# Kernel optimization log

Measured on AMD Instinct MI355X. Metric: run time of the kernel, lower is better.

The kernel has to match this reference:

```python
import jax, jax.numpy as jnp
import numpy as np

BEV_H = 200
BEV_W = 200
H_METERS = 100.0
W_METERS = 100.0
THRESHOLD = 0.05
LOW_PASS = 0.3  # 3DGS screen-space low-pass filter added to cov2D diagonal
ALPHA_MIN = 1.0 / 255.0
ALPHA_MAX = 0.99


def setup_inputs() -> dict:
    key = jax.random.key(0)
    k1, k2, k3, k4 = jax.random.split(key, 4)
    B, G, D = 2, 2000, 32
    features = jax.random.normal(k1, (B, G, D), dtype=jnp.float32)
    # means uniformly covering the [-50, 50] x [-50, 50] BEV extent (z unused)
    means3D = (jax.random.uniform(k2, (B, G, 3), dtype=jnp.float32) - 0.5) * 100.0
    # PSD 3x3 covariances, ~1-2 m std -> a few pixels at 2 px/m
    A = jax.random.normal(k3, (B, G, 3, 3), dtype=jnp.float32)
    Sigma = jnp.einsum('bgij,bgkj->bgik', A, A) + 0.1 * jnp.eye(3, dtype=jnp.float32)
    iu = jnp.triu_indices(3)
    cov3D = Sigma[:, :, iu[0], iu[1]]  # b g 6 : (xx, xy, xz, yy, yz, zz)
    opacities = jax.random.uniform(k4, (B, G, 1), dtype=jnp.float32)
    return {'features': features, 'means3D': means3D, 'cov3D': cov3D,
            'opacities': opacities}


def _render(features, means3D, cov3D, opacities):
    B, G, D = features.shape
    sh = BEV_H / H_METERS  # 2 px / m
    sw = BEV_W / W_METERS
    op = opacities[..., 0]                      # b g
    mask = op > THRESHOLD                       # opacity gating (torch masks rows;
                                                # zero-alpha is mathematically identical)
    # orthographic BEV projection (full_proj_transform rows 0 and 1)
    x, y = means3D[..., 0], means3D[..., 1]
    u = -sh * y + BEV_H / 2.0                   # row coordinate, b g
    v = -sw * x + BEV_W / 2.0                   # col coordinate, b g
    # cov2D = M Sigma M^T with M = [[0, sh, 0], [sw, 0, 0]], plus low-pass
    sxx, sxy, syy = cov3D[..., 0], cov3D[..., 1], cov3D[..., 3]
    c00 = sh * sh * syy + LOW_PASS
    c01 = sh * sw * sxy
    c11 = sw * sw * sxx + LOW_PASS
    det = c00 * c11 - c01 * c01
    valid = mask & (det > 0.0)
    inv_det = jnp.where(det > 0.0, 1.0 / jnp.where(det > 0.0, det, 1.0), 0.0)
    cA = c11 * inv_det                          # conic (A, B, C)
    cB = -c01 * inv_det
    cC = c00 * inv_det
    # per-pixel Gaussian power, separably broadcast: [b g H 1] + [b g 1 W]
    gi = jnp.arange(BEV_H, dtype=jnp.float32)
    gj = jnp.arange(BEV_W, dtype=jnp.float32)
    du = u[..., None] - gi                      # b g H
    dv = v[..., None] - gj                      # b g W
    power = (-0.5 * cA)[..., None, None] * (du * du)[..., :, None] \
          + (-0.5 * cC)[..., None, None] * (dv * dv)[..., None, :] \
          + (-cB)[..., None, None] * du[..., :, None] * dv[..., None, :]  # b g H W
    alpha = jnp.minimum(ALPHA_MAX, op[..., None, None] * jnp.exp(power))
    keep = valid[..., None, None] & (power <= 0.0) & (alpha >= ALPHA_MIN)
    alpha = jnp.where(keep, alpha, 0.0)
    alpha = alpha.reshape(B, G, BEV_H * BEV_W)  # b g p
    # front-to-back alpha compositing: exclusive cumprod of transmittance
    T_excl = jnp.concatenate(
        [jnp.ones((B, 1, BEV_H * BEV_W), dtype=alpha.dtype),
         jnp.cumprod(1.0 - alpha, axis=1)[:, :-1]], axis=1)
    weight = alpha * T_excl                     # b g p
    out = jnp.einsum('bgp,bgd->bdp', weight, features)  # bg_color is zeros
    out = out.reshape(B, D, BEV_H, BEV_W)
    num_gaussians = jnp.mean(jnp.sum(mask.astype(jnp.float32), axis=1))
    return out, num_gaussians


def reference(features, means3D, cov3D, opacities):
    return _render(features, means3D, cov3D, opacities)
```

## Files before the change

### kernel.cpp

```cpp
#include <hip/hip_runtime.h>
#include <math.h>

#define BEV_H 200
#define BEV_W 200
#define NPIX (BEV_H * BEV_W)
#define TILE 8
#define NT 25
#define NB 2
#define T_DEAD 1e-10f
#define SEGCAP 512
#define PCAP 128
#define KC 32
#define NLOG255 (-5.5412635f)

__device__ __forceinline__ unsigned pk2bf(float x, float y)
{
    unsigned ux = __float_as_uint(x), uy = __float_as_uint(y);
    ux = ux + 0x7fffu + ((ux >> 16) & 1u);
    uy = uy + 0x7fffu + ((uy >> 16) & 1u);
    return (ux >> 16) | (uy & 0xffff0000u);
}

__global__ __launch_bounds__(256, 5) void render_fused_kernel(
    const float* __restrict__ features, const float* __restrict__ means3D,
    const float* __restrict__ cov3D, const float* __restrict__ opac,
    float* __restrict__ out, int G)
{
    __shared__ __align__(16) unsigned char smem[24576];
    unsigned short* glist = (unsigned short*)smem;
    float4* plA = (float4*)(smem + 4096);
    float2* plB = (float2*)(smem + 12288);
    uint4*  flq = (uint4*)(smem + 16384);
    float*  xch = (float*)smem;

    const int tid  = threadIdx.x;
    const int lane = tid & 63;
    const int w    = tid >> 6;
    const int b  = blockIdx.z;
    const int tj = blockIdx.x;
    const int ti = blockIdx.y;
    const int j = tj * TILE + (lane & 7);
    const int i = ti * TILE + (lane >> 3);
    const float fi = (float)i, fj = (float)j;
    const float ti_lo = (float)(ti * TILE), ti_hi = ti_lo + (TILE - 1);
    const float tj_lo = (float)(tj * TILE), tj_hi = tj_lo + (TILE - 1);
    const int gbase = b * G;
    const int g_lo = (w * G) >> 2;
    const int g_hi = ((w + 1) * G) >> 2;
    const int rounds = (g_hi - g_lo + 63) >> 6;

    int tot = 0;
    {
        int gg = min(g_lo + lane, g_hi - 1);
        size_t gi = (size_t)(gbase + gg);
        float x0 = means3D[gi * 3 + 0], y0 = means3D[gi * 3 + 1];
        float s0 = cov3D[gi * 6 + 0], s1 = cov3D[gi * 6 + 1], s3 = cov3D[gi * 6 + 3];
        float o0 = opac[gi];
        for (int r = 0; r < rounds; ++r) {
            float x1 = 0.f, y1 = 0.f, t0 = 0.f, t1 = 0.f, t3 = 0.f, o1 = 0.f;
            if (r + 1 < rounds) {
                const int gn = min(g_lo + (r + 1) * 64 + lane, g_hi - 1);
                const size_t gni = (size_t)(gbase + gn);
                x1 = means3D[gni * 3 + 0]; y1 = means3D[gni * 3 + 1];
                t0 = cov3D[gni * 6 + 0];   t1 = cov3D[gni * 6 + 1];
                t3 = cov3D[gni * 6 + 3];   o1 = opac[gni];
            }
            const int g = g_lo + r * 64 + lane;
            const float u = -2.0f * y0 + 100.0f;
            const float v = -2.0f * x0 + 100.0f;
            const float c00 = 4.0f * s3 + 0.3f;
            const float c01 = 4.0f * s1;
            const float c11 = 4.0f * s0 + 0.3f;
            const float det = c00 * c11 - c01 * c01;
            bool keep = false;
            float L = 0.0f;
            if (o0 > 0.05f && det > 0.0f && g < g_hi) {
                L = __logf(255.0f * o0);
                const float ru = sqrtf(2.0f * L * c00) + 0.01f;
                const float rv = sqrtf(2.0f * L * c11) + 0.01f;
                keep = (u + ru >= ti_lo) && (u - ru <= ti_hi) &&
                       (v + rv >= tj_lo) && (v - rv <= tj_hi);
            }
            const unsigned long long bal = __ballot(keep);
            if (keep) {
                const int slot = tot + (int)__popcll(bal & ((1ull << lane) - 1ull));
                glist[w * SEGCAP + slot] = (unsigned short)g;
                if (slot < PCAP) {
                    const float inv = 1.0f / det;
                    plA[w * PCAP + slot] =
                        make_float4(u, v, -0.5f * c11 * inv, c01 * inv);
                    plB[w * PCAP + slot] = make_float2(-0.5f * c00 * inv,
                                                       L + NLOG255);
                }
            }
            tot += (int)__popcll(bal);
            x0 = x1; y0 = y1; s0 = t0; s1 = t1; s3 = t3; o0 = o1;
        }
    }

    float acc[32];
#pragma unroll
    for (int d = 0; d < 32; ++d) acc[d] = 0.0f;
    float T = 1.0f;

    for (int k0 = 0; k0 < tot; k0 += KC) {
        if (!__any(T >= T_DEAD)) break;
        const int nk = min(KC, tot - k0);

        if (k0 >= PCAP && lane < nk) {
            const int g = glist[w * SEGCAP + k0 + lane];
            const size_t gi = (size_t)(gbase + g);
            const float x = means3D[gi * 3 + 0], y = means3D[gi * 3 + 1];
            const float sxx = cov3D[gi * 6 + 0], sxy = cov3D[gi * 6 + 1],
                        syy = cov3D[gi * 6 + 3];
            const float op = opac[gi];
            const float u = -2.0f * y + 100.0f;
            const float v = -2.0f * x + 100.0f;
            const float c00 = 4.0f * syy + 0.3f;
            const float c01 = 4.0f * sxy;
            const float c11 = 4.0f * sxx + 0.3f;
            const float inv = 1.0f / (c00 * c11 - c01 * c01);
            plA[w * PCAP + lane] = make_float4(u, v, -0.5f * c11 * inv, c01 * inv);
            plB[w * PCAP + lane] = make_float2(-0.5f * c00 * inv, __logf(op));
        }
        for (int idx = lane; idx < nk * 4; idx += 64) {
            const int e = idx >> 2, q = idx & 3;
            const int g = glist[w * SEGCAP + k0 + e];
            const float4* fp =
                (const float4*)(features + (size_t)(gbase + g) * 32) + q * 2;
            const float4 A = fp[0], Bq = fp[1];
            flq[(w * KC + e) * 4 + q] = make_uint4(pk2bf(A.x, A.y), pk2bf(A.z, A.w),
                                                   pk2bf(Bq.x, Bq.y), pk2bf(Bq.z, Bq.w));
        }

        const int pbase = w * PCAP + ((k0 < PCAP) ? k0 : 0);
        for (int k = 0; k < nk; ++k) {
            const float4 pA = plA[pbase + k];
            const float2 pB = plB[pbase + k];
            const float du = pA.x - fi;
            const float dv = pA.y - fj;
            const float power = pA.z * du * du + pB.x * dv * dv + pA.w * du * dv;
            const float powb = power + pB.y;
            float alpha = fminf(0.99f, __expf(powb));
            const bool ok = (powb >= NLOG255) && (power <= 0.0f);
            alpha = ok ? alpha : 0.0f;
            const float wgt = alpha * T;
            T *= 1.0f - alpha;
#pragma unroll
            for (int q = 0; q < 4; ++q) {
                const uint4 uq = flq[(w * KC + k) * 4 + q];
                const unsigned uu[4] = {uq.x, uq.y, uq.z, uq.w};
#pragma unroll
                for (int c = 0; c < 4; ++c) {
                    const float lo = __uint_as_float(uu[c] << 16);
                    const float hi = __uint_as_float(uu[c] & 0xffff0000u);
                    acc[q * 8 + c * 2 + 0] = fmaf(wgt, lo, acc[q * 8 + c * 2 + 0]);
                    acc[q * 8 + c * 2 + 1] = fmaf(wgt, hi, acc[q * 8 + c * 2 + 1]);
                }
            }
        }
    }

    __syncthreads();
    if (w == 1 || w == 3) {
        float* row = xch + (((w - 1) >> 1) * 64 + lane) * 33;
#pragma unroll
        for (int d = 0; d < 32; ++d) row[d] = acc[d];
        row[32] = T;
    }
    __syncthreads();
    if (w == 0 || w == 2) {
        const float* row = xch + ((w >> 1) * 64 + lane) * 33;
        const float Tn = row[32];
#pragma unroll
        for (int d = 0; d < 32; ++d) acc[d] = fmaf(T, row[d], acc[d]);
        T *= Tn;
    }
    __syncthreads();
    if (w == 2) {
        float* row = xch + lane * 33;
#pragma unroll
        for (int d = 0; d < 32; ++d) row[d] = acc[d];
        row[32] = T;
    }
    __syncthreads();

    if (w == 0) {
        const float* row = xch + lane * 33;
#pragma unroll
        for (int d = 0; d < 32; ++d) acc[d] = fmaf(T, row[d], acc[d]);

        const int p = i * BEV_W + j;
        float* ob = out + (size_t)b * 32 * NPIX + p;
#pragma unroll
        for (int d = 0; d < 32; ++d) ob[(size_t)d * NPIX] = acc[d];
    }

    if (w == 1 && blockIdx.x == 0 && blockIdx.y == 0 && blockIdx.z == 0) {
        const float4* o4 = (const float4*)opac;
        const int n4 = (NB * G) >> 2;
        float s = 0.0f;
        for (int idx = lane; idx < n4; idx += 64) {
            const float4 o = o4[idx];
            s += (o.x > 0.05f ? 1.0f : 0.0f) + (o.y > 0.05f ? 1.0f : 0.0f) +
                 (o.z > 0.05f ? 1.0f : 0.0f) + (o.w > 0.05f ? 1.0f : 0.0f);
        }
#pragma unroll
        for (int off = 32; off > 0; off >>= 1) s += __shfl_down(s, off);
        if (lane == 0) out[NB * 32 * NPIX] = s * (1.0f / NB);
    }
}

extern "C" void kernel_launch(void* const* d_in, const int* in_sizes, int n_in,
                              void* d_out, int out_size, void* d_ws, size_t ws_size,
                              hipStream_t stream)
{
    const float* features = (const float*)d_in[0];
    const float* means3D  = (const float*)d_in[1];
    const float* cov3D    = (const float*)d_in[2];
    const float* opac     = (const float*)d_in[3];
    float* out = (float*)d_out;

    const int G = in_sizes[3] / NB;

    dim3 grid(NT, NT, NB);
    render_fused_kernel<<<grid, 256, 0, stream>>>(features, means3D, cov3D, opac,
                                                  out, G);
}
```

Baseline: 82.44 us.

## Precompute Gaussian params and per-tile bitmasks in a separate binning kernel

Adds a binning kernel that computes each Gaussian's conic parameters once and sets bits in per-tile bitmask words with atomicOr. The render kernel then builds its per-wave Gaussian list by expanding 16 mask words instead of having every tile scan all G Gaussians. Parameters are read from the precomputed buffer, which removes the redundant per-tile recomputation and the PCAP shared cache. In exchange it adds a memset, a second launch, atomics and a workspace dependency. Wave w maps to Gaussians w*512..w*512+511, which assumes G <= 2048.

```diff
diff --git a/kernel.cpp b/kernel.cpp
--- a/kernel.cpp
+++ b/kernel.cpp
@@ -9,8 +9,8 @@
 #define NB 2
 #define T_DEAD 1e-10f
 #define SEGCAP 512
-#define PCAP 128
 #define KC 32
+#define MWORDS 64
 #define NLOG255 (-5.5412635f)
 
 __device__ __forceinline__ unsigned pk2bf(float x, float y)
@@ -21,16 +21,55 @@
     return (ux >> 16) | (uy & 0xffff0000u);
 }
 
-__global__ __launch_bounds__(256, 5) void render_fused_kernel(
-    const float* __restrict__ features, const float* __restrict__ means3D,
-    const float* __restrict__ cov3D, const float* __restrict__ opac,
+__global__ __launch_bounds__(256) void bin_kernel(
+    const float* __restrict__ means3D, const float* __restrict__ cov3D,
+    const float* __restrict__ opac, float4* __restrict__ params,
+    unsigned* __restrict__ masks, int G, int n)
+{
+    const int idx = blockIdx.x * 256 + threadIdx.x;
+    if (idx >= n) return;
+    const int b = idx / G;
+    const int g = idx - b * G;
+    const float x = means3D[idx * 3 + 0], y = means3D[idx * 3 + 1];
+    const float sxx = cov3D[idx * 6 + 0], sxy = cov3D[idx * 6 + 1],
+                syy = cov3D[idx * 6 + 3];
+    const float op = opac[idx];
+    const float u = -2.0f * y + 100.0f;
+    const float v = -2.0f * x + 100.0f;
+    const float c00 = 4.0f * syy + 0.3f;
+    const float c01 = 4.0f * sxy;
+    const float c11 = 4.0f * sxx + 0.3f;
+    const float det = c00 * c11 - c01 * c01;
+    if (!(op > 0.05f && det > 0.0f)) return;
+    const float inv = 1.0f / det;
+    const float L = __logf(255.0f * op);
+    params[(size_t)idx * 2 + 0] = make_float4(u, v, -0.5f * c11 * inv, c01 * inv);
+    params[(size_t)idx * 2 + 1] = make_float4(-0.5f * c00 * inv, L + NLOG255,
+                                              0.0f, 0.0f);
+    const float ru = sqrtf(2.0f * L * c00) + 0.01f;
+    const float rv = sqrtf(2.0f * L * c11) + 0.01f;
+    const int ti0 = max(0, (int)ceilf((u - ru - 7.001f) * 0.125f));
+    const int ti1 = min(NT - 1, (int)floorf((u + ru + 0.001f) * 0.125f));
+    const int tj0 = max(0, (int)ceilf((v - rv - 7.001f) * 0.125f));
+    const int tj1 = min(NT - 1, (int)floorf((v + rv + 0.001f) * 0.125f));
+    const int word = g >> 5;
+    const unsigned bit = 1u << (g & 31);
+    for (int ti = ti0; ti <= ti1; ++ti)
+        for (int tj = tj0; tj <= tj1; ++tj)
+            atomicOr(&masks[(size_t)(((b * NT) + ti) * NT + tj) * MWORDS + word],
+                     bit);
+}
+
+__global__ __launch_bounds__(256, 5) void render_tile_kernel(
+    const float* __restrict__ features, const float4* __restrict__ params,
+    const unsigned* __restrict__ masks, const float* __restrict__ opac,
     float* __restrict__ out, int G)
 {
-    __shared__ __align__(16) unsigned char smem[24576];
+    __shared__ __align__(16) unsigned char smem[16896];
     unsigned short* glist = (unsigned short*)smem;
     float4* plA = (float4*)(smem + 4096);
-    float2* plB = (float2*)(smem + 12288);
-    uint4*  flq = (uint4*)(smem + 16384);
+    float2* plB = (float2*)(smem + 6144);
+    uint4*  flq = (uint4*)(smem + 7168);
     float*  xch = (float*)smem;
 
     const int tid  = threadIdx.x;
@@ -42,60 +81,22 @@
     const int j = tj * TILE + (lane & 7);
     const int i = ti * TILE + (lane >> 3);
     const float fi = (float)i, fj = (float)j;
-    const float ti_lo = (float)(ti * TILE), ti_hi = ti_lo + (TILE - 1);
-    const float tj_lo = (float)(tj * TILE), tj_hi = tj_lo + (TILE - 1);
     const int gbase = b * G;
-    const int g_lo = (w * G) >> 2;
-    const int g_hi = ((w + 1) * G) >> 2;
-    const int rounds = (g_hi - g_lo + 63) >> 6;
-
+
+    const size_t mbase = (size_t)(((b * NT) + ti) * NT + tj) * MWORDS + w * 16;
+    const unsigned m = (lane < 16) ? masks[mbase + lane] : 0u;
     int tot = 0;
-    {
-        int gg = min(g_lo + lane, g_hi - 1);
-        size_t gi = (size_t)(gbase + gg);
-        float x0 = means3D[gi * 3 + 0], y0 = means3D[gi * 3 + 1];
-        float s0 = cov3D[gi * 6 + 0], s1 = cov3D[gi * 6 + 1], s3 = cov3D[gi * 6 + 3];
-        float o0 = opac[gi];
-        for (int r = 0; r < rounds; ++r) {
-            float x1 = 0.f, y1 = 0.f, t0 = 0.f, t1 = 0.f, t3 = 0.f, o1 = 0.f;
-            if (r + 1 < rounds) {
-                const int gn = min(g_lo + (r + 1) * 64 + lane, g_hi - 1);
-                const size_t gni = (size_t)(gbase + gn);
-                x1 = means3D[gni * 3 + 0]; y1 = means3D[gni * 3 + 1];
-                t0 = cov3D[gni * 6 + 0];   t1 = cov3D[gni * 6 + 1];
-                t3 = cov3D[gni * 6 + 3];   o1 = opac[gni];
-            }
-            const int g = g_lo + r * 64 + lane;
-            const float u = -2.0f * y0 + 100.0f;
-            const float v = -2.0f * x0 + 100.0f;
-            const float c00 = 4.0f * s3 + 0.3f;
-            const float c01 = 4.0f * s1;
-            const float c11 = 4.0f * s0 + 0.3f;
-            const float det = c00 * c11 - c01 * c01;
-            bool keep = false;
-            float L = 0.0f;
-            if (o0 > 0.05f && det > 0.0f && g < g_hi) {
-                L = __logf(255.0f * o0);
-                const float ru = sqrtf(2.0f * L * c00) + 0.01f;
-                const float rv = sqrtf(2.0f * L * c11) + 0.01f;
-                keep = (u + ru >= ti_lo) && (u - ru <= ti_hi) &&
-                       (v + rv >= tj_lo) && (v - rv <= tj_hi);
-            }
-            const unsigned long long bal = __ballot(keep);
-            if (keep) {
-                const int slot = tot + (int)__popcll(bal & ((1ull << lane) - 1ull));
-                glist[w * SEGCAP + slot] = (unsigned short)g;
-                if (slot < PCAP) {
-                    const float inv = 1.0f / det;
-                    plA[w * PCAP + slot] =
-                        make_float4(u, v, -0.5f * c11 * inv, c01 * inv);
-                    plB[w * PCAP + slot] = make_float2(-0.5f * c00 * inv,
-                                                       L + NLOG255);
-                }
-            }
-            tot += (int)__popcll(bal);
-            x0 = x1; y0 = y1; s0 = t0; s1 = t1; s3 = t3; o0 = o1;
-        }
+#pragma unroll
+    for (int r = 0; r < 8; ++r) {
+        const unsigned lo = __shfl(m, 2 * r);
+        const unsigned hi = __shfl(m, 2 * r + 1);
+        const unsigned long long mm = ((unsigned long long)hi << 32) | lo;
+        if ((mm >> lane) & 1ull) {
+            const int pre = (int)__popcll(mm & ((1ull << lane) - 1ull));
+            glist[w * SEGCAP + tot + pre] =
+                (unsigned short)(w * 512 + r * 64 + lane);
+        }
+        tot += (int)__popcll(mm);
     }
 
     float acc[32];
@@ -107,21 +108,13 @@
         if (!__any(T >= T_DEAD)) break;
         const int nk = min(KC, tot - k0);
 
-        if (k0 >= PCAP && lane < nk) {
+        if (lane < nk) {
             const int g = glist[w * SEGCAP + k0 + lane];
-            const size_t gi = (size_t)(gbase + g);
-            const float x = means3D[gi * 3 + 0], y = means3D[gi * 3 + 1];
-            const float sxx = cov3D[gi * 6 + 0], sxy = cov3D[gi * 6 + 1],
-                        syy = cov3D[gi * 6 + 3];
-            const float op = opac[gi];
-            const float u = -2.0f * y + 100.0f;
-            const float v = -2.0f * x + 100.0f;
-            const float c00 = 4.0f * syy + 0.3f;
-            const float c01 = 4.0f * sxy;
-            const float c11 = 4.0f * sxx + 0.3f;
-            const float inv = 1.0f / (c00 * c11 - c01 * c01);
-            plA[w * PCAP + lane] = make_float4(u, v, -0.5f * c11 * inv, c01 * inv);
-            plB[w * PCAP + lane] = make_float2(-0.5f * c00 * inv, __logf(op));
+            const float4* pp = params + (size_t)(gbase + g) * 2;
+            const float4 a = pp[0];
+            const float4 c = pp[1];
+            plA[w * KC + lane] = a;
+            plB[w * KC + lane] = make_float2(c.x, c.y);
         }
         for (int idx = lane; idx < nk * 4; idx += 64) {
             const int e = idx >> 2, q = idx & 3;
@@ -129,14 +122,14 @@
             const float4* fp =
                 (const float4*)(features + (size_t)(gbase + g) * 32) + q * 2;
             const float4 A = fp[0], Bq = fp[1];
-            flq[(w * KC + e) * 4 + q] = make_uint4(pk2bf(A.x, A.y), pk2bf(A.z, A.w),
-                                                   pk2bf(Bq.x, Bq.y), pk2bf(Bq.z, Bq.w));
-        }
-
-        const int pbase = w * PCAP + ((k0 < PCAP) ? k0 : 0);
+            flq[(w * KC + e) * 4 + q] =
+                make_uint4(pk2bf(A.x, A.y), pk2bf(A.z, A.w),
+                           pk2bf(Bq.x, Bq.y), pk2bf(Bq.z, Bq.w));
+        }
+
         for (int k = 0; k < nk; ++k) {
-            const float4 pA = plA[pbase + k];
-            const float2 pB = plB[pbase + k];
+            const float4 pA = plA[w * KC + k];
+            const float2 pB = plB[w * KC + k];
             const float du = pA.x - fi;
             const float dv = pA.y - fj;
             const float power = pA.z * du * du + pB.x * dv * dv + pA.w * du * dv;
@@ -152,10 +145,10 @@
                 const unsigned uu[4] = {uq.x, uq.y, uq.z, uq.w};
 #pragma unroll
                 for (int c = 0; c < 4; ++c) {
-                    const float lo = __uint_as_float(uu[c] << 16);
-                    const float hi = __uint_as_float(uu[c] & 0xffff0000u);
-                    acc[q * 8 + c * 2 + 0] = fmaf(wgt, lo, acc[q * 8 + c * 2 + 0]);
-                    acc[q * 8 + c * 2 + 1] = fmaf(wgt, hi, acc[q * 8 + c * 2 + 1]);
+                    const float lof = __uint_as_float(uu[c] << 16);
+                    const float hif = __uint_as_float(uu[c] & 0xffff0000u);
+                    acc[q * 8 + c * 2 + 0] = fmaf(wgt, lof, acc[q * 8 + c * 2 + 0]);
+                    acc[q * 8 + c * 2 + 1] = fmaf(wgt, hif, acc[q * 8 + c * 2 + 1]);
                 }
             }
         }
@@ -222,8 +215,18 @@
     float* out = (float*)d_out;
 
     const int G = in_sizes[3] / NB;
+    const int n = NB * G;
+
+    const size_t mask_bytes = (size_t)NB * NT * NT * MWORDS * 4;
+    unsigned* masks = (unsigned*)d_ws;
+    float4* params  = (float4*)((char*)d_ws + mask_bytes);
+
+    hipMemsetAsync(masks, 0, mask_bytes, stream);
+
+    bin_kernel<<<(n + 255) / 256, 256, 0, stream>>>(
+        means3D, cov3D, opac, params, masks, G, n);
 
     dim3 grid(NT, NT, NB);
-    render_fused_kernel<<<grid, 256, 0, stream>>>(features, means3D, cov3D, opac,
-                                                  out, G);
-}
+    render_tile_kernel<<<grid, 256, 0, stream>>>(features, params, masks, opac,
+                                                 out, G);
+}
```

New measurement: 85.99 us. 4.3% more time.
